# Kernel tuning notes

Measured on AMD Instinct MI355X. Metric: run time of the kernel, lower is better.

## Reference

```python
import jax, jax.numpy as jnp
import numpy as np
from jax import lax

RADIUS = 2
DILATION = 2

def _mind_kernels():
    # 6-neighbourhood offsets within a 3x3x3 stencil
    six = np.array([[0, 1, 1], [1, 1, 0], [1, 0, 1], [1, 1, 2], [2, 1, 1], [1, 2, 1]], dtype=np.int64)
    # pairwise squared distances between the 6 offsets
    dist = ((six[:, None, :] - six[None, :, :]) ** 2).sum(-1)  # [6,6]
    i, j = np.meshgrid(np.arange(6), np.arange(6), indexing='ij')
    mask = ((i > j) & (dist == 2)).ravel()  # 12 True entries
    idx1 = six[np.repeat(np.arange(6), 6)][mask]  # [12,3]
    idx2 = six[np.tile(np.arange(6), 6)][mask]    # [12,3]
    m1 = np.zeros((12, 1, 3, 3, 3), np.float32)
    m2 = np.zeros((12, 1, 3, 3, 3), np.float32)
    m1[np.arange(12), 0, idx1[:, 0], idx1[:, 1], idx1[:, 2]] = 1.0
    m2[np.arange(12), 0, idx2[:, 0], idx2[:, 1], idx2[:, 2]] = 1.0
    return jnp.asarray(m1), jnp.asarray(m2)

MSHIFT1, MSHIFT2 = _mind_kernels()

def _rep_pad(x, p):
    # ReplicationPad3d on NCDHW
    return jnp.pad(x, ((0, 0), (0, 0), (p, p), (p, p), (p, p)), mode='edge')

def _shift_conv(x, w):
    # Conv3d(1->12, k=3, stride=1, padding=1, dilation=DILATION, bias=False)
    return lax.conv_general_dilated(
        x, w, window_strides=(1, 1, 1),
        padding=((1, 1), (1, 1), (1, 1)),
        rhs_dilation=(DILATION, DILATION, DILATION),
        dimension_numbers=('NCDHW', 'OIDHW', 'NCDHW'))

def _avg_pool3d(x, k):
    s = lax.reduce_window(x, jnp.float32(0.0), lax.add,
                          (1, 1, k, k, k), (1, 1, 1, 1, 1), 'VALID')
    return s / jnp.float32(k ** 3)

def mind3d(x):
    xp = _rep_pad(x, DILATION)
    diff = _shift_conv(xp, MSHIFT1) - _shift_conv(xp, MSHIFT2)  # [B,12,D+2,H+2,W+2]
    ssd = _avg_pool3d(_rep_pad(diff * diff, RADIUS), 2 * RADIUS + 1)
    mind = ssd - jnp.min(ssd, axis=1, keepdims=True)
    mind_var = jnp.mean(mind, axis=1, keepdims=True)  # [B,1,...]
    mv_mean = jnp.mean(mind_var)
    mind_var = jnp.clip(mind_var, mv_mean * 0.001, mv_mean * 1000.0)
    return jnp.exp(-mind / mind_var)

def setup_inputs() -> dict:
    key = jax.random.key(0)
    x = jax.random.uniform(key, (1, 1, 128, 128, 128), dtype=jnp.float32)
    return {"x": x}

def reference(x):
    return mind3d(x)
```

## Files before the change

kernel.cpp:

```cpp
#include <hip/hip_runtime.h>
#include <math.h>

#define N    130
#define NN   (130*130)
#define NNN  (130*130*130)
#define NQ4  (NNN/4)
#define NCH  12
#define XN   128
#define XNN  (XN*XN)

#define WT   9
#define HT   11
#define DSEGS 13
#define STEPS 14

typedef float f32x4 __attribute__((ext_vector_type(4)));

__global__ __launch_bounds__(256) void k_fused(const float* __restrict__ x,
                                               float* __restrict__ Cout,
                                               float* __restrict__ MV,
                                               double* __restrict__ acc) {
    const int tid = threadIdx.x;
    const int wl  = tid & 15;
    const int r   = tid >> 4;

    const int b    = blockIdx.x;
    const int wt   = b % WT;
    const int rest = b / WT;
    const int ht   = rest % HT;
    const int ds   = rest / HT;

    const int W0 = wt * 16;
    const int H0 = ht * 12;
    const int D0 = ds * 10;

    const int  w_out = W0 + wl;
    const int  wc    = min(w_out, 129);
    const int  ghW   = min(max(H0 - 2 + r, 0), 129);
    const int  oh    = H0 + r - 2;
    const bool interior = (r >= 2) && (r < 14);
    const bool valid    = interior && (oh < N) && (w_out < N);

    const int   ih_c = min(max(ghW - 1, 0), 127);
    const int   ih_m = min(max(ghW - 3, 0), 127);
    const int   ih_p = min(ghW + 1, 127);
    const float fhm  = (ghW >= 1)   ? 1.0f : 0.0f;
    const float fhp  = (ghW <= 128) ? 1.0f : 0.0f;
    const int   dhm  = (ih_m - ih_c) * XN;
    const int   dhp  = (ih_p - ih_c) * XN;

    int   oc[5], o4[5], o5[5];
    float fwm[5], fwp[5];
    #pragma unroll
    for (int j = 0; j < 5; ++j) {
        const int cw = min(max(wc + j - 2, 0), 129);
        oc[j] = ih_c * XN + min(max(cw - 1, 0), 127);
        o4[j] = ih_c * XN + min(max(cw - 3, 0), 127);
        o5[j] = ih_c * XN + min(cw + 1, 127);
        fwm[j] = (cw >= 1)   ? 1.0f : 0.0f;
        fwp[j] = (cw <= 128) ? 1.0f : 0.0f;
    }

    __shared__ f32x4 Wlds[2][3][16][16];
    __shared__ float red[256];

    f32x4 ring[5][3];
    float lsum   = 0.0f;
    int   voxoff = D0 * NN + oh * N + w_out;

    float PF[5];
    float fdpP;

#define PRE(IT) do {                                                          \
    const int bdn = D0 - 2 + (IT);                                            \
    const int dcn = min(max(bdn, 0), 129);                                    \
    const float* ppn = x + (size_t)(min(dcn + 1, 127)) * XNN;                 \
    fdpP = (dcn <= 128) ? 1.0f : 0.0f;                                        \
    _Pragma("unroll") for (int j = 0; j < 5; ++j) PF[j] = ppn[oc[j]];         \
} while (0)

#define STEP(IT, SLOT, DOUT) do {                                             \
    const int it_ = (IT);                                                     \
    const int bd = D0 - 2 + it_;                                              \
    const int dc = min(max(bd, 0), 129);                                      \
    const float* pc = x + (size_t)(min(max(dc - 1, 0), 127)) * XNN;           \
    const float* pm = x + (size_t)(min(max(dc - 3, 0), 127)) * XNN;           \
    const float fdm = (dc >= 1)   ? 1.0f : 0.0f;                              \
                     \
    const float fdp_ = fdpP;                                                  \
    float y1v[5];                                                             \
    _Pragma("unroll") for (int j = 0; j < 5; ++j) y1v[j] = PF[j] * fdp_;      \
    PRE(it_ + 1);                            \
    float Wa[12];                                                             \
    _Pragma("unroll") for (int z = 0; z < 12; ++z) Wa[z] = 0.0f;              \
    _Pragma("unroll") for (int j = 0; j < 5; ++j) {                           \
        const float y0 = pm[oc[j]]       * fdm;                               \
        const float y1 = y1v[j];                                              \
        const float y2 = pc[oc[j] + dhm] * fhm;                               \
        const float y3 = pc[oc[j] + dhp] * fhp;                               \
        const float y4 = pc[o4[j]]       * fwm[j];                            \
        const float y5 = pc[o5[j]]       * fwp[j];                            \
        float t;                                                              \
        t = y4 - y0; Wa[0]  += t * t;  t = y2 - y0; Wa[1]  += t * t;          \
        t = y2 - y4; Wa[2]  += t * t;  t = y5 - y0; Wa[3]  += t * t;          \
        t = y5 - y2; Wa[4]  += t * t;  t = y1 - y4; Wa[5]  += t * t;          \
        t = y1 - y2; Wa[6]  += t * t;  t = y1 - y5; Wa[7]  += t * t;          \
        t = y3 - y0; Wa[8]  += t * t;  t = y3 - y4; Wa[9]  += t * t;          \
        t = y3 - y5; Wa[10] += t * t;  t = y3 - y1; Wa[11] += t * t;          \
    }                                                                         \
    const int pb = it_ & 1;                                                   \
    Wlds[pb][0][r][wl] = (f32x4){Wa[0], Wa[1], Wa[2],  Wa[3]};                \
    Wlds[pb][1][r][wl] = (f32x4){Wa[4], Wa[5], Wa[6],  Wa[7]};                \
    Wlds[pb][2][r][wl] = (f32x4){Wa[8], Wa[9], Wa[10], Wa[11]};               \
     \
    asm volatile("s_waitcnt lgkmcnt(0)" ::: "memory");                        \
    __builtin_amdgcn_s_barrier();                                             \
    if (interior) {                                                           \
        _Pragma("unroll") for (int g = 0; g < 3; ++g) {                       \
            f32x4 a = Wlds[pb][g][r - 2][wl];                                 \
            a += Wlds[pb][g][r - 1][wl];                                      \
            a += Wlds[pb][g][r    ][wl];                                      \
            a += Wlds[pb][g][r + 1][wl];                                      \
            a += Wlds[pb][g][r + 2][wl];                                      \
            ring[SLOT][g] = a;                                                \
        }                                                                     \
        if (DOUT) {                                                           \
            f32x4 sg[3];                                                      \
            _Pragma("unroll") for (int g = 0; g < 3; ++g) {                   \
                f32x4 a = ring[0][g];                                         \
                a += ring[1][g]; a += ring[2][g];                             \
                a += ring[3][g]; a += ring[4][g];                             \
                sg[g] = a * (1.0f / 125.0f);                                  \
            }                                                                 \
            float sv[12];                                                     \
            _Pragma("unroll") for (int g = 0; g < 3; ++g) {                   \
                sv[4*g+0] = sg[g].x; sv[4*g+1] = sg[g].y;                     \
                sv[4*g+2] = sg[g].z; sv[4*g+3] = sg[g].w;                     \
            }                                                                 \
            float mn = sv[0], tt = sv[0];                                     \
            _Pragma("unroll") for (int z = 1; z < 12; ++z) {                  \
                mn = fminf(mn, sv[z]); tt += sv[z];                           \
            }                                                                 \
            if (valid) {                                                      \
                const float mvar = tt * (1.0f / 12.0f) - mn;                  \
                const float inv  = 1.0f / fmaxf(mvar, 1e-20f);                \
                _Pragma("unroll") for (int z = 0; z < 12; ++z)                \
                    Cout[(size_t)z * NNN + (unsigned)voxoff] =                \
                        __expf(-(sv[z] - mn) * inv);                          \
                MV[(unsigned)voxoff] = mvar;                                  \
                lsum += mvar;                                                 \
                voxoff += NN;                                                 \
            }                                                                 \
        }                                                                     \
    }                                                                         \
} while (0)

    PRE(0);
    STEP(0, 0, false);
    STEP(1, 1, false);
    STEP(2, 2, false);
    STEP(3, 3, false);

    STEP(4, 4, true);  STEP(5, 0, true);  STEP(6, 1, true);
    STEP(7, 2, true);  STEP(8, 3, true);
    STEP(9, 4, true);  STEP(10, 0, true); STEP(11, 1, true);
    STEP(12, 2, true); STEP(13, 3, true);
#undef STEP
#undef PRE

    red[tid] = lsum;
    __syncthreads();
    for (int st = 128; st > 0; st >>= 1) {
        if (tid < st) red[tid] += red[tid + st];
        __syncthreads();
    }
    if (tid == 0) atomicAdd(acc, (double)red[0]);
}

__global__ void k_zero(double* acc) {
    if (blockIdx.x == 0 && threadIdx.x == 0) *acc = 0.0;
}

__global__ __launch_bounds__(256) void k_fix(float* __restrict__ io,
                                             const float* __restrict__ MV,
                                             const double* __restrict__ acc) {
    const float mv_mean = (float)(*acc * (1.0 / (double)NNN));
    const float lo = mv_mean * 0.001f, hi = mv_mean * 1000.0f;
    for (int q = blockIdx.x * 256 + threadIdx.x; q < NQ4;
         q += gridDim.x * 256) {
        const f32x4 mv = *((const f32x4*)MV + q);
        #pragma unroll
        for (int k = 0; k < 4; ++k) {
            const float used = fmaxf(mv[k], 1e-20f);
            const float cl   = fminf(fmaxf(mv[k], lo), hi);
            const float e    = used / cl;
            if (fabsf(e - 1.0f) > 1e-6f) {
                const size_t vox = (size_t)q * 4 + k;
                #pragma unroll
                for (int o = 0; o < NCH; ++o) {
                    const float v = io[(size_t)o * NNN + vox];
                    if (v > 0.0f)
                        io[(size_t)o * NNN + vox] = __powf(v, e);
                }
            }
        }
    }
}

extern "C" void kernel_launch(void* const* d_in, const int* in_sizes, int n_in,
                              void* d_out, int out_size, void* d_ws, size_t ws_size,
                              hipStream_t stream) {
    const float* x = (const float*)d_in[0];
    float* out = (float*)d_out;
    float* MV  = (float*)d_ws;
    double* acc = (double*)((char*)d_ws + (size_t)NNN * sizeof(float));

    k_zero <<<1, 64, 0, stream>>>(acc);
    k_fused<<<WT * HT * DSEGS, 256, 0, stream>>>(x, out, MV, acc);
    k_fix  <<<1024, 256, 0, stream>>>(out, MV, acc);
}
```

Measured before the change: 187.3 us.

## Use DPP lane sums for W-window, remap blocks across XCDs, skip fix pass

The W-direction 5-tap box sum is now done with DPP cross-lane adds instead of each thread recomputing five columns. This cuts global loads and FMAs about fivefold but shrinks the useful width per tile from 16 to 12, so more blocks are launched. Block indices are remapped so that neighbouring tiles land on the same XCD, which should improve L2 reuse. The fused kernel also records global min and max of the variance, letting the fix kernel exit early when no clamping is needed, at the cost of two extra block reductions and atomics.

Measured after the change: 184.7 us. No clear change (-1.4%).

```diff
diff --git a/kernel.cpp b/kernel.cpp
--- a/kernel.cpp
+++ b/kernel.cpp
@@ -9,110 +9,107 @@
 #define XN   128
 #define XNN  (XN*XN)
 
-#define WT   9
+#define WT   11
 #define HT   11
 #define DSEGS 13
-#define STEPS 14
+#define NWG  (WT*HT*DSEGS)
 
 typedef float f32x4 __attribute__((ext_vector_type(4)));
+
+template <int CTRL>
+__device__ __forceinline__ float dppf(float v) {
+    return __int_as_float(__builtin_amdgcn_update_dpp(
+        0, __float_as_int(v), CTRL, 0xF, 0xF, true));
+}
+#define W5(v) ((v) + dppf<0x111>(v) + dppf<0x112>(v) \
+                   + dppf<0x101>(v) + dppf<0x102>(v))
 
 __global__ __launch_bounds__(256) void k_fused(const float* __restrict__ x,
                                                float* __restrict__ Cout,
                                                float* __restrict__ MV,
-                                               double* __restrict__ acc) {
+                                               double* __restrict__ acc,
+                                               unsigned* __restrict__ gmm) {
     const int tid = threadIdx.x;
     const int wl  = tid & 15;
     const int r   = tid >> 4;
 
-    const int b    = blockIdx.x;
+    const int qq  = NWG >> 3, rm = NWG & 7;
+    const int xcd = blockIdx.x & 7, idx = blockIdx.x >> 3;
+    const int b   = (xcd < rm ? xcd * (qq + 1)
+                              : rm * (qq + 1) + (xcd - rm) * qq) + idx;
+
     const int wt   = b % WT;
     const int rest = b / WT;
     const int ht   = rest % HT;
     const int ds   = rest / HT;
 
-    const int W0 = wt * 16;
+    const int W0 = wt * 12;
     const int H0 = ht * 12;
     const int D0 = ds * 10;
 
-    const int  w_out = W0 + wl;
-    const int  wc    = min(w_out, 129);
-    const int  ghW   = min(max(H0 - 2 + r, 0), 129);
-    const int  oh    = H0 + r - 2;
+    const int  w_gl = W0 + wl - 2;
+    const int  bw   = min(max(w_gl, 0), 129);
+    const int  ghW  = min(max(H0 - 2 + r, 0), 129);
+    const int  oh   = H0 + r - 2;
     const bool interior = (r >= 2) && (r < 14);
-    const bool valid    = interior && (oh < N) && (w_out < N);
+    const bool validw   = (wl >= 2) && (wl < 14) && (w_gl < N);
+    const bool valid    = interior && (oh < N) && validw;
 
     const int   ih_c = min(max(ghW - 1, 0), 127);
-    const int   ih_m = min(max(ghW - 3, 0), 127);
-    const int   ih_p = min(ghW + 1, 127);
     const float fhm  = (ghW >= 1)   ? 1.0f : 0.0f;
     const float fhp  = (ghW <= 128) ? 1.0f : 0.0f;
-    const int   dhm  = (ih_m - ih_c) * XN;
-    const int   dhp  = (ih_p - ih_c) * XN;
-
-    int   oc[5], o4[5], o5[5];
-    float fwm[5], fwp[5];
-    #pragma unroll
-    for (int j = 0; j < 5; ++j) {
-        const int cw = min(max(wc + j - 2, 0), 129);
-        oc[j] = ih_c * XN + min(max(cw - 1, 0), 127);
-        o4[j] = ih_c * XN + min(max(cw - 3, 0), 127);
-        o5[j] = ih_c * XN + min(cw + 1, 127);
-        fwm[j] = (cw >= 1)   ? 1.0f : 0.0f;
-        fwp[j] = (cw <= 128) ? 1.0f : 0.0f;
-    }
+    const int   dhm  = (min(max(ghW - 3, 0), 127) - ih_c) * XN;
+    const int   dhp  = (min(ghW + 1, 127)        - ih_c) * XN;
+
+    const int   col_c = ih_c * XN + min(max(bw - 1, 0), 127);
+    const int   col_m = ih_c * XN + min(max(bw - 3, 0), 127);
+    const int   col_p = ih_c * XN + min(bw + 1, 127);
+    const float fw_m  = (bw >= 1)   ? 1.0f : 0.0f;
+    const float fw_p  = (bw <= 128) ? 1.0f : 0.0f;
 
     __shared__ f32x4 Wlds[2][3][16][16];
     __shared__ float red[256];
 
     f32x4 ring[5][3];
-    float lsum   = 0.0f;
-    int   voxoff = D0 * NN + oh * N + w_out;
-
-    float PF[5];
-    float fdpP;
+    float lsum  = 0.0f;
+    float mn_mv = INFINITY, mx_mv = 0.0f;
+    int   voxoff = D0 * NN + oh * N + (valid ? w_gl : 0);
+
+    float PF, fdpP;
 
 #define PRE(IT) do {                                                          \
-    const int bdn = D0 - 2 + (IT);                                            \
-    const int dcn = min(max(bdn, 0), 129);                                    \
-    const float* ppn = x + (size_t)(min(dcn + 1, 127)) * XNN;                 \
+    const int dcn = min(max(D0 - 2 + (IT), 0), 129);                          \
+    PF   = x[(size_t)(min(dcn + 1, 127)) * XNN + col_c];                      \
     fdpP = (dcn <= 128) ? 1.0f : 0.0f;                                        \
-    _Pragma("unroll") for (int j = 0; j < 5; ++j) PF[j] = ppn[oc[j]];         \
 } while (0)
 
 #define STEP(IT, SLOT, DOUT) do {                                             \
     const int it_ = (IT);                                                     \
-    const int bd = D0 - 2 + it_;                                              \
-    const int dc = min(max(bd, 0), 129);                                      \
+    const int dc  = min(max(D0 - 2 + it_, 0), 129);                           \
     const float* pc = x + (size_t)(min(max(dc - 1, 0), 127)) * XNN;           \
     const float* pm = x + (size_t)(min(max(dc - 3, 0), 127)) * XNN;           \
-    const float fdm = (dc >= 1)   ? 1.0f : 0.0f;                              \
-                     \
-    const float fdp_ = fdpP;                                                  \
-    float y1v[5];                                                             \
-    _Pragma("unroll") for (int j = 0; j < 5; ++j) y1v[j] = PF[j] * fdp_;      \
-    PRE(it_ + 1);                            \
+    const float fdm = (dc >= 1) ? 1.0f : 0.0f;                                \
+    const float y1 = PF * fdpP;                    \
+    PRE(it_ + 1);                             \
+    const float y0 = pm[col_c]       * fdm;                                   \
+    const float y2 = pc[col_c + dhm] * fhm;                                   \
+    const float y3 = pc[col_c + dhp] * fhp;                                   \
+    const float y4 = pc[col_m]       * fw_m;                                  \
+    const float y5 = pc[col_p]       * fw_p;                                  \
     float Wa[12];                                                             \
-    _Pragma("unroll") for (int z = 0; z < 12; ++z) Wa[z] = 0.0f;              \
-    _Pragma("unroll") for (int j = 0; j < 5; ++j) {                           \
-        const float y0 = pm[oc[j]]       * fdm;                               \
-        const float y1 = y1v[j];                                              \
-        const float y2 = pc[oc[j] + dhm] * fhm;                               \
-        const float y3 = pc[oc[j] + dhp] * fhp;                               \
-        const float y4 = pc[o4[j]]       * fwm[j];                            \
-        const float y5 = pc[o5[j]]       * fwp[j];                            \
-        float t;                                                              \
-        t = y4 - y0; Wa[0]  += t * t;  t = y2 - y0; Wa[1]  += t * t;          \
-        t = y2 - y4; Wa[2]  += t * t;  t = y5 - y0; Wa[3]  += t * t;          \
-        t = y5 - y2; Wa[4]  += t * t;  t = y1 - y4; Wa[5]  += t * t;          \
-        t = y1 - y2; Wa[6]  += t * t;  t = y1 - y5; Wa[7]  += t * t;          \
-        t = y3 - y0; Wa[8]  += t * t;  t = y3 - y4; Wa[9]  += t * t;          \
-        t = y3 - y5; Wa[10] += t * t;  t = y3 - y1; Wa[11] += t * t;          \
-    }                                                                         \
+    { float t;                                                                \
+      t = y4 - y0; Wa[0]  = t * t;  t = y2 - y0; Wa[1]  = t * t;              \
+      t = y2 - y4; Wa[2]  = t * t;  t = y5 - y0; Wa[3]  = t * t;              \
+      t = y5 - y2; Wa[4]  = t * t;  t = y1 - y4; Wa[5]  = t * t;              \
+      t = y1 - y2; Wa[6]  = t * t;  t = y1 - y5; Wa[7]  = t * t;              \
+      t = y3 - y0; Wa[8]  = t * t;  t = y3 - y4; Wa[9]  = t * t;              \
+      t = y3 - y5; Wa[10] = t * t;  t = y3 - y1; Wa[11] = t * t; }            \
+    _Pragma("unroll") for (int z = 0; z < 12; ++z) Wa[z] = W5(Wa[z]);         \
     const int pb = it_ & 1;                                                   \
     Wlds[pb][0][r][wl] = (f32x4){Wa[0], Wa[1], Wa[2],  Wa[3]};                \
     Wlds[pb][1][r][wl] = (f32x4){Wa[4], Wa[5], Wa[6],  Wa[7]};                \
     Wlds[pb][2][r][wl] = (f32x4){Wa[8], Wa[9], Wa[10], Wa[11]};               \
-     \
+       \
     asm volatile("s_waitcnt lgkmcnt(0)" ::: "memory");                        \
     __builtin_amdgcn_s_barrier();                                             \
     if (interior) {                                                           \
@@ -149,6 +146,8 @@
                         __expf(-(sv[z] - mn) * inv);                          \
                 MV[(unsigned)voxoff] = mvar;                                  \
                 lsum += mvar;                                                 \
+                mn_mv = fminf(mn_mv, mvar);                                   \
+                mx_mv = fmaxf(mx_mv, mvar);                                   \
                 voxoff += NN;                                                 \
             }                                                                 \
         }                                                                     \
@@ -160,7 +159,6 @@
     STEP(1, 1, false);
     STEP(2, 2, false);
     STEP(3, 3, false);
-
     STEP(4, 4, true);  STEP(5, 0, true);  STEP(6, 1, true);
     STEP(7, 2, true);  STEP(8, 3, true);
     STEP(9, 4, true);  STEP(10, 0, true); STEP(11, 1, true);
@@ -175,17 +173,41 @@
         __syncthreads();
     }
     if (tid == 0) atomicAdd(acc, (double)red[0]);
-}
-
-__global__ void k_zero(double* acc) {
-    if (blockIdx.x == 0 && threadIdx.x == 0) *acc = 0.0;
+    __syncthreads();
+    red[tid] = mn_mv;
+    __syncthreads();
+    for (int st = 128; st > 0; st >>= 1) {
+        if (tid < st) red[tid] = fminf(red[tid], red[tid + st]);
+        __syncthreads();
+    }
+    if (tid == 0) atomicMin(&gmm[0], __float_as_uint(red[0]));
+    __syncthreads();
+    red[tid] = mx_mv;
+    __syncthreads();
+    for (int st = 128; st > 0; st >>= 1) {
+        if (tid < st) red[tid] = fmaxf(red[tid], red[tid + st]);
+        __syncthreads();
+    }
+    if (tid == 0) atomicMax(&gmm[1], __float_as_uint(red[0]));
+}
+
+__global__ void k_zero(double* acc, unsigned* gmm) {
+    if (blockIdx.x == 0 && threadIdx.x == 0) {
+        *acc = 0.0;
+        gmm[0] = 0xFFFFFFFFu;
+        gmm[1] = 0u;
+    }
 }
 
 __global__ __launch_bounds__(256) void k_fix(float* __restrict__ io,
                                              const float* __restrict__ MV,
-                                             const double* __restrict__ acc) {
+                                             const double* __restrict__ acc,
+                                             const unsigned* __restrict__ gmm) {
     const float mv_mean = (float)(*acc * (1.0 / (double)NNN));
     const float lo = mv_mean * 0.001f, hi = mv_mean * 1000.0f;
+    const float gmin = __uint_as_float(gmm[0]);
+    const float gmax = __uint_as_float(gmm[1]);
+    if (gmin >= lo && gmax <= hi) return;
     for (int q = blockIdx.x * 256 + threadIdx.x; q < NQ4;
          q += gridDim.x * 256) {
         const f32x4 mv = *((const f32x4*)MV + q);
@@ -213,9 +235,10 @@
     const float* x = (const float*)d_in[0];
     float* out = (float*)d_out;
     float* MV  = (float*)d_ws;
-    double* acc = (double*)((char*)d_ws + (size_t)NNN * sizeof(float));
-
-    k_zero <<<1, 64, 0, stream>>>(acc);
-    k_fused<<<WT * HT * DSEGS, 256, 0, stream>>>(x, out, MV, acc);
-    k_fix  <<<1024, 256, 0, stream>>>(out, MV, acc);
-}
+    double*  acc = (double*)((char*)d_ws + (size_t)NNN * sizeof(float));
+    unsigned* gmm = (unsigned*)((char*)d_ws + (size_t)NNN * sizeof(float) + 8);
+
+    k_zero <<<1, 64, 0, stream>>>(acc, gmm);
+    k_fused<<<NWG, 256, 0, stream>>>(x, out, MV, acc, gmm);
+    k_fix  <<<1024, 256, 0, stream>>>(out, MV, acc, gmm);
+}
```
